# Kernel optimization log

Measured on AMD Instinct MI355X. Metric: run time of the kernel, lower is better.

## Reference

```python
import jax, jax.numpy as jnp
import numpy as np

B, N, DIM, H, DH = 8, 1024, 1024, 16, 64

def setup_inputs() -> dict:
    key = jax.random.key(0)
    ks = jax.random.split(key, 6)
    return {
        'x': jax.random.normal(ks[0], (B, N, DIM), dtype=jnp.float32),
        'freqs': jax.random.normal(ks[1], (1, N, DH), dtype=jnp.float32),
        'bias': jax.random.normal(ks[2], (1, N, DH), dtype=jnp.float32),
        'ln_gamma': jnp.ones((DIM,), jnp.float32),
        'ln_beta': jnp.zeros((DIM,), jnp.float32),
        'w_qk': jax.random.normal(ks[3], (DIM, 2 * H * DH), dtype=jnp.float32) * (DIM ** -0.5),
        'w_v': jax.random.normal(ks[4], (DIM, H * DH), dtype=jnp.float32) * (DIM ** -0.5),
        'w_out': jax.random.normal(ks[5], (H * DH, DIM), dtype=jnp.float32) * ((H * DH) ** -0.5),
        'b_out': jnp.zeros((DIM,), jnp.float32),
    }

def _apply_polar(t, freqs):
    # t: [b,h,n,d]; freqs: [1,n,d] broadcast over b,h. Output doubles last dim.
    t = jax.nn.softplus(t)
    return jnp.concatenate((t * jnp.cos(freqs), t * jnp.sin(freqs)), axis=-1)

def reference(x, freqs, bias, ln_gamma, ln_beta, w_qk, w_v, w_out, b_out):
    eps = 1e-5
    mu = jnp.mean(x, axis=-1, keepdims=True)
    var = jnp.var(x, axis=-1, keepdims=True)
    xn = (x - mu) * jax.lax.rsqrt(var + eps) * ln_gamma + ln_beta
    qk = jnp.einsum('bnd,de->bne', xn, w_qk)
    q, k = jnp.split(qk, 2, axis=-1)
    v = jnp.einsum('bnd,de->bne', xn, w_v)
    split_heads = lambda t: t.reshape(B, N, H, DH).transpose(0, 2, 1, 3)
    q, k, v = split_heads(q), split_heads(k), split_heads(v)
    q = _apply_polar(q, freqs)          # [b,h,n,2*DH]
    k = _apply_polar(k, freqs + bias)   # [b,h,n,2*DH]
    scale = DH ** -0.5
    dots = jnp.einsum('bhnd,bhmd->bhnm', q, k) * scale
    attn = jax.nn.softmax(dots, axis=-1)
    out = jnp.einsum('bhnm,bhmd->bhnd', attn, v)
    out = out.transpose(0, 2, 1, 3).reshape(B, N, H * DH)
    return jnp.einsum('bne,ed->bnd', out, w_out) + b_out
```

## Files before the change

### kernel.cpp

```cpp
#include <hip/hip_runtime.h>
#include <cmath>

using f16   = _Float16;
using f16x2 = __attribute__((ext_vector_type(2))) _Float16;
using f16x4 = __attribute__((ext_vector_type(4))) _Float16;
using f16x8 = __attribute__((ext_vector_type(8))) _Float16;
using f32x4 = __attribute__((ext_vector_type(4))) float;

#define DEV __device__ __forceinline__

constexpr int Bb  = 8;
constexpr int Nn  = 1024;
constexpr int DIM = 1024;
constexpr int Hh  = 16;
constexpr int DH  = 64;
constexpr int EQKV = 3072;

DEV void async16(const f16* g, f16* l) {
  __builtin_amdgcn_global_load_lds(
      (const __attribute__((address_space(1))) void*)g,
      (__attribute__((address_space(3))) void*)l, 16, 0, 0);
}

DEV float softplusf(float x) {
  return fmaxf(x, 0.f) + __logf(1.f + __expf(-fabsf(x)));
}

__global__ __launch_bounds__(256) void transpose_cvt3(const float* __restrict__ s0,
                                                      const float* __restrict__ s1,
                                                      const float* __restrict__ s2,
                                                      f16* __restrict__ d0,
                                                      f16* __restrict__ d2) {
  __shared__ float tile[32][33];
  const float* src; f16* dst; int cols;
  int bz = blockIdx.z;
  if (bz == 0)      { src = s0; dst = d0;                        cols = 2048; }
  else if (bz == 1) { src = s1; dst = d0 + (size_t)2048 * 1024;  cols = 1024; }
  else              { src = s2; dst = d2;                        cols = 1024; }
  int c0 = blockIdx.x * 32, r0 = blockIdx.y * 32;
  if (c0 >= cols) return;
  int t = threadIdx.x, tx = t & 31, ty = t >> 5;
#pragma unroll
  for (int j = 0; j < 32; j += 8)
    tile[ty + j][tx] = src[(size_t)(r0 + ty + j) * cols + c0 + tx];
  __syncthreads();
#pragma unroll
  for (int j = 0; j < 32; j += 8)
    dst[(size_t)(c0 + ty + j) * 1024 + r0 + tx] = (f16)tile[tx][ty + j];
}

__global__ __launch_bounds__(256) void ln_kernel(const float* __restrict__ x,
                                                 const float* __restrict__ gamma,
                                                 const float* __restrict__ beta,
                                                 f16* __restrict__ xn) {
  int row = blockIdx.x;
  int t = threadIdx.x;
  const float4* xr = (const float4*)(x + (size_t)row * DIM);
  float4 v = xr[t];
  float s  = v.x + v.y + v.z + v.w;
  float s2 = v.x * v.x + v.y * v.y + v.z * v.z + v.w * v.w;
#pragma unroll
  for (int off = 32; off; off >>= 1) {
    s  += __shfl_xor(s,  off, 64);
    s2 += __shfl_xor(s2, off, 64);
  }
  __shared__ float red[8];
  int wv = t >> 6, lane = t & 63;
  if (lane == 0) { red[wv] = s; red[4 + wv] = s2; }
  __syncthreads();
  s  = red[0] + red[1] + red[2] + red[3];
  s2 = red[4] + red[5] + red[6] + red[7];
  float mu  = s * (1.f / DIM);
  float var = s2 * (1.f / DIM) - mu * mu;
  float rs  = rsqrtf(var + 1e-5f);
  float4 g = ((const float4*)gamma)[t];
  float4 bb = ((const float4*)beta)[t];
  f16x4 o;
  o[0] = (f16)((v.x - mu) * rs * g.x + bb.x);
  o[1] = (f16)((v.y - mu) * rs * g.y + bb.y);
  o[2] = (f16)((v.z - mu) * rs * g.z + bb.z);
  o[3] = (f16)((v.w - mu) * rs * g.w + bb.w);
  ((f16x4*)(xn + (size_t)row * DIM))[t] = o;
}

template <bool FP32OUT>
__global__ __launch_bounds__(256) void gemm_bt(const f16* __restrict__ A,
                                               const f16* __restrict__ Bt,
                                               void* __restrict__ Cv,
                                               const float* __restrict__ bias,
                                               int M, int K, int E) {
  __shared__ f16 lA[128 * 32];
  __shared__ f16 lB[128 * 32];
  int tid  = threadIdx.x;
  int lane = tid & 63;
  int wv   = __builtin_amdgcn_readfirstlane(tid >> 6);
  int nbe  = E >> 7;
  int bm = blockIdx.x / nbe, be = blockIdx.x % nbe;
  size_t m0 = (size_t)bm * 128, e0 = (size_t)be * 128;
  int wm = (wv & 1) * 64, we = (wv >> 1) * 64;
  int lm = lane & 15, q = lane >> 4;

  f32x4 acc[4][4] = {};

  int row_s[2], cg_s[2];
#pragma unroll
  for (int r = 0; r < 2; ++r) {
    int s = r * 256 + tid;
    row_s[r] = s >> 2;
    cg_s[r]  = (s & 3) ^ ((row_s[r] >> 1) & 3);
  }
  const f16* pa[4];
  const f16* pb[4];
#pragma unroll
  for (int i = 0; i < 4; ++i) {
    int ra = wm + i * 16 + lm;
    pa[i] = lA + ra * 32 + (q ^ ((ra >> 1) & 3)) * 8;
    int rb = we + i * 16 + lm;
    pb[i] = lB + rb * 32 + (q ^ ((rb >> 1) & 3)) * 8;
  }

  for (int k0 = 0; k0 < K; k0 += 32) {
#pragma unroll
    for (int r = 0; r < 2; ++r) {
      const f16* ga = A  + (m0 + row_s[r]) * K + k0 + cg_s[r] * 8;
      const f16* gb = Bt + (e0 + row_s[r]) * K + k0 + cg_s[r] * 8;
      async16(ga, lA + (r * 256 + wv * 64) * 8);
      async16(gb, lB + (r * 256 + wv * 64) * 8);
    }
    __syncthreads();
    f16x8 af[4], bf[4];
#pragma unroll
    for (int i = 0; i < 4; ++i) {
      af[i] = *(const f16x8*)pa[i];
      bf[i] = *(const f16x8*)pb[i];
    }
#pragma unroll
    for (int i = 0; i < 4; ++i)
#pragma unroll
      for (int j = 0; j < 4; ++j)
        acc[i][j] = __builtin_amdgcn_mfma_f32_16x16x32_f16(af[i], bf[j], acc[i][j], 0, 0, 0);
    __syncthreads();
  }

#pragma unroll
  for (int i = 0; i < 4; ++i) {
    size_t mbase = m0 + wm + i * 16 + q * 4;
#pragma unroll
    for (int j = 0; j < 4; ++j) {
      size_t e = e0 + we + j * 16 + lm;
#pragma unroll
      for (int g = 0; g < 4; ++g) {
        float val = acc[i][j][g];
        if (FP32OUT)
          ((float*)Cv)[(mbase + g) * (size_t)E + e] = val + bias[e];
        else
          ((f16*)Cv)[(mbase + g) * (size_t)E + e] = (f16)val;
      }
    }
  }
}

template <bool FP32OUT>
__global__ __launch_bounds__(512, 2) void gemm256(const f16* __restrict__ A,
                                                  const f16* __restrict__ Bt,
                                                  void* __restrict__ Cv,
                                                  const float* __restrict__ bias,
                                                  int M, int K, int E) {
  __shared__ f16 sm[65536];
  const int tid  = threadIdx.x;
  const int lane = tid & 63;
  const int wv   = __builtin_amdgcn_readfirstlane(tid >> 6);
  const int lm   = lane & 15, q = lane >> 4;
  const int wrow = (wv >> 2) * 128;
  const int wcol = (wv & 3) * 64;

  const int nbe = E >> 8;
  const int cpx = gridDim.x >> 3;
  const int bid = blockIdx.x;
  const int swz = (bid & 7) * cpx + (bid >> 3);
  const int bm = swz / nbe, be = swz % nbe;
  const size_t m0 = (size_t)bm * 256, e0 = (size_t)be * 256;

  const int rl  = lane >> 3;
  const int pcp = lane & 7;
  const int cg  = pcp ^ rl;
  const f16* aS = A  + (m0 + (size_t)(wv * 8 + rl)) * K + cg * 8;
  const f16* bS = Bt + (e0 + (size_t)((wv >> 2) * 64 + (wv & 3) * 8 + rl)) * K + cg * 8;
  const int aDofs = wv * 512;
  const int bDofs = 16384 + ((wv >> 2) * 64 + (wv & 3) * 8) * 64;

  const int x0 = ((0 + q) ^ (lm & 7)) * 8;
  const int x1 = ((4 + q) ^ (lm & 7)) * 8;

  const int NT = K >> 6;

  async16(aS,                     sm + aDofs);
  async16(aS + (size_t)64 * K,    sm + aDofs + 64 * 64);
  async16(aS + (size_t)128 * K,   sm + aDofs + 128 * 64);
  async16(aS + (size_t)192 * K,   sm + aDofs + 192 * 64);
  async16(bS,                     sm + bDofs);
  async16(bS + (size_t)32 * K,    sm + bDofs + 32 * 64);
  async16(bS + (size_t)128 * K,   sm + bDofs + 128 * 64);
  async16(bS + (size_t)160 * K,   sm + bDofs + 160 * 64);

  f32x4 acc[8][4] = {};
  f16x8 af[4][2], bf[4][2];

  for (int t = 0; t < NT; ++t) {
    const int b = t & 1, nb = b ^ 1;
    const int tn = (t + 1 < NT) ? t + 1 : t;
    const f16* pA = sm + b * 32768;
    const f16* pB = pA + 16384;
    f16* aD = sm + nb * 32768 + aDofs;
    f16* bD = sm + nb * 32768 + bDofs;
    const f16* aSk = aS + tn * 64;
    const f16* bSk = bS + tn * 64;

    __builtin_amdgcn_s_barrier();

    async16(aSk,                   aD);
    async16(aSk + (size_t)64 * K,  aD + 64 * 64);
    async16(aSk + (size_t)128 * K, aD + 128 * 64);
    async16(aSk + (size_t)192 * K, aD + 192 * 64);
    async16(bSk,                   bD);
    async16(bSk + (size_t)32 * K,  bD + 32 * 64);
    async16(bSk + (size_t)128 * K, bD + 128 * 64);
    async16(bSk + (size_t)160 * K, bD + 160 * 64);

    asm volatile("s_waitcnt vmcnt(8)" ::: "memory");
    __builtin_amdgcn_s_barrier();

#pragma unroll
    for (int i = 0; i < 4; ++i) {
      const f16* p = pA + (wrow + i * 16 + lm) * 64;
      af[i][0] = *(const f16x8*)(p + x0);
      af[i][1] = *(const f16x8*)(p + x1);
    }
#pragma unroll
    for (int j = 0; j < 2; ++j) {
      const f16* p = pB + (wcol + j * 16 + lm) * 64;
      bf[j][0] = *(const f16x8*)(p + x0);
      bf[j][1] = *(const f16x8*)(p + x1);
    }
    __builtin_amdgcn_s_setprio(1);
#pragma unroll
    for (int i = 0; i < 4; ++i)
#pragma unroll
      for (int j = 0; j < 2; ++j) {
        acc[i][j] = __builtin_amdgcn_mfma_f32_16x16x32_f16(af[i][0], bf[j][0], acc[i][j], 0, 0, 0);
        acc[i][j] = __builtin_amdgcn_mfma_f32_16x16x32_f16(af[i][1], bf[j][1], acc[i][j], 0, 0, 0);
      }
    __builtin_amdgcn_s_setprio(0);
    __builtin_amdgcn_s_barrier();

#pragma unroll
    for (int j = 0; j < 2; ++j) {
      const f16* p = pB + (wcol + 32 + j * 16 + lm) * 64;
      bf[2 + j][0] = *(const f16x8*)(p + x0);
      bf[2 + j][1] = *(const f16x8*)(p + x1);
    }
    __builtin_amdgcn_s_setprio(1);
#pragma unroll
    for (int i = 0; i < 4; ++i)
#pragma unroll
      for (int j = 2; j < 4; ++j) {
        acc[i][j] = __builtin_amdgcn_mfma_f32_16x16x32_f16(af[i][0], bf[j][0], acc[i][j], 0, 0, 0);
        acc[i][j] = __builtin_amdgcn_mfma_f32_16x16x32_f16(af[i][1], bf[j][1], acc[i][j], 0, 0, 0);
      }
    __builtin_amdgcn_s_setprio(0);
    __builtin_amdgcn_s_barrier();

#pragma unroll
    for (int i = 0; i < 4; ++i) {
      const f16* p = pA + (wrow + 64 + i * 16 + lm) * 64;
      af[i][0] = *(const f16x8*)(p + x0);
      af[i][1] = *(const f16x8*)(p + x1);
    }
    __builtin_amdgcn_s_setprio(1);
#pragma unroll
    for (int i = 0; i < 4; ++i)
#pragma unroll
      for (int j = 0; j < 2; ++j) {
        acc[4 + i][j] = __builtin_amdgcn_mfma_f32_16x16x32_f16(af[i][0], bf[j][0], acc[4 + i][j], 0, 0, 0);
        acc[4 + i][j] = __builtin_amdgcn_mfma_f32_16x16x32_f16(af[i][1], bf[j][1], acc[4 + i][j], 0, 0, 0);
      }
    __builtin_amdgcn_s_setprio(0);
    __builtin_amdgcn_s_barrier();

    __builtin_amdgcn_s_setprio(1);
#pragma unroll
    for (int i = 0; i < 4; ++i)
#pragma unroll
      for (int j = 2; j < 4; ++j) {
        acc[4 + i][j] = __builtin_amdgcn_mfma_f32_16x16x32_f16(af[i][0], bf[j][0], acc[4 + i][j], 0, 0, 0);
        acc[4 + i][j] = __builtin_amdgcn_mfma_f32_16x16x32_f16(af[i][1], bf[j][1], acc[4 + i][j], 0, 0, 0);
      }
    __builtin_amdgcn_s_setprio(0);
  }
  asm volatile("s_waitcnt vmcnt(0)" ::: "memory");

#pragma unroll
  for (int ii = 0; ii < 8; ++ii) {
    size_t mrow = m0 + wrow + (ii >> 2) * 64 + (ii & 3) * 16 + q * 4;
#pragma unroll
    for (int j = 0; j < 4; ++j) {
      size_t e = e0 + wcol + j * 16 + lm;
#pragma unroll
      for (int g = 0; g < 4; ++g) {
        float val = acc[ii][j][g];
        if (FP32OUT)
          ((float*)Cv)[(mrow + g) * (size_t)E + e] = val + bias[e];
        else
          ((f16*)Cv)[(mrow + g) * (size_t)E + e] = (f16)val;
      }
    }
  }
}

__global__ __launch_bounds__(256) void polar_kernel(const f16* __restrict__ qkv,
                                                    const float* __restrict__ freqs,
                                                    const float* __restrict__ fbias,
                                                    f16* __restrict__ Qp,
                                                    f16* __restrict__ Kp,
                                                    f16* __restrict__ Vt) {
  __shared__ f16 vt[64 * 66];
  int tid = threadIdx.x;
  int bx = blockIdx.x;
  int nt = bx & 15, bh = bx >> 4;
  int b = bh >> 4, h = bh & 15;
  size_t tok0 = (size_t)b * Nn + nt * 64;
  int n0 = nt * 64;
  constexpr float kScale = 0.125f;
#pragma unroll
  for (int i = 0; i < 8; ++i) {
    int e2 = tid + i * 256;
    int nl = e2 >> 5, dp = (e2 & 31) * 2;
    size_t src = (tok0 + nl) * EQKV + h * 64 + dp;
    f16x2 q2 = *(const f16x2*)(qkv + src);
    f16x2 k2 = *(const f16x2*)(qkv + src + 1024);
    f16x2 v2 = *(const f16x2*)(qkv + src + 2048);
    int fidx = (n0 + nl) * 64 + dp;
    float2 f2  = *(const float2*)(freqs + fidx);
    float2 fb2 = *(const float2*)(fbias + fidx);
    f16x2 qc, qs, kc, ksn;
#pragma unroll
    for (int u = 0; u < 2; ++u) {
      float fq = u ? f2.y : f2.x;
      float fk = fq + (u ? fb2.y : fb2.x);
      float spq = softplusf((float)q2[u]) * kScale;
      float spk = softplusf((float)k2[u]);
      float snq, csq, snk, csk;
      __sincosf(fq, &snq, &csq);
      __sincosf(fk, &snk, &csk);
      qc[u]  = (f16)(spq * csq);
      qs[u]  = (f16)(spq * snq);
      kc[u]  = (f16)(spk * csk);
      ksn[u] = (f16)(spk * snk);
    }
    size_t dst = ((size_t)bh * Nn + n0 + nl) * 128 + dp;
    *(f16x2*)(Qp + dst)      = qc;
    *(f16x2*)(Qp + dst + 64) = qs;
    *(f16x2*)(Kp + dst)      = kc;
    *(f16x2*)(Kp + dst + 64) = ksn;
    vt[dp * 66 + nl]       = v2[0];
    vt[(dp + 1) * 66 + nl] = v2[1];
  }
  __syncthreads();
#pragma unroll
  for (int i = 0; i < 16; ++i) {
    int e = tid + i * 256;
    int d = e >> 6, nl = e & 63;
    Vt[((size_t)bh * 64 + d) * Nn + n0 + nl] = vt[d * 66 + nl];
  }
}

constexpr int VK0 = 0;
constexpr int VK1 = 8192;
constexpr int VV0 = 16384;
constexpr int VV1 = 21504;
constexpr int VEND = 26624;

__global__ __launch_bounds__(256, 3) void attn_kernel(const f16* __restrict__ Qp,
                                                      const f16* __restrict__ Kp,
                                                      const f16* __restrict__ Vt,
                                                      f16* __restrict__ attout) {
  __shared__ f16 smem[VEND];

  int tid = threadIdx.x, lane = tid & 63;
  int wv = __builtin_amdgcn_readfirstlane(tid >> 6);
  int lm = lane & 15, q = lane >> 4;
  int bx = blockIdx.x;
  int bh = (bx & 7) | ((bx >> 6) << 3);
  int qt = (bx >> 3) & 7;
  const f16* Kbase = Kp + (size_t)bh * Nn * 128;
  const f16* Vbase = Vt + (size_t)bh * 64 * Nn;

  {
    int idx = tid * 4;
    f16 val = (idx < 64) ? (f16)1.0f : (f16)0.0f;
    f16x4 v4 = {val, val, val, val};
    *(f16x4*)(smem + VV0 + 64 * 64 + idx) = v4;
    *(f16x4*)(smem + VV1 + 64 * 64 + idx) = v4;
  }

#pragma unroll
  for (int i = 0; i < 4; ++i) {
    int s = i * 256 + tid;
    int r = s >> 4, c = s & 15;
    int g = c ^ (r & 15);
    async16(Kbase + (size_t)r * 128 + g * 8, smem + VK0 + (i * 256 + wv * 64) * 8);
  }
#pragma unroll
  for (int i = 0; i < 2; ++i) {
    int s = i * 256 + tid;
    int r = s >> 3, c = s & 7;
    int g = c ^ (r & 7);
    async16(Vbase + (size_t)r * Nn + g * 8, smem + VV0 + (i * 256 + wv * 64) * 8);
  }

  f16x8 qf[2][4];
  {
    const f16* Qb = Qp + ((size_t)bh * Nn + qt * 128 + wv * 32) * 128;
#pragma unroll
    for (int grp = 0; grp < 2; ++grp)
#pragma unroll
      for (int ks = 0; ks < 4; ++ks)
        qf[grp][ks] = *(const f16x8*)(Qb + (size_t)(grp * 16 + lm) * 128 + ks * 32 + q * 8);
  }

  f32x4 O[2][5] = {};
  float mrow[2] = {-INFINITY, -INFINITY};

  for (int kt = 0; kt < 16; ++kt) {
    __syncthreads();

    if (kt < 15) {
      f16* nK = smem + ((kt & 1) ? VK0 : VK1);
      f16* nV = smem + ((kt & 1) ? VV0 : VV1);
#pragma unroll
      for (int i = 0; i < 4; ++i) {
        int s = i * 256 + tid;
        int r = s >> 4, c = s & 15;
        int g = c ^ (r & 15);
        async16(Kbase + (size_t)((kt + 1) * 64 + r) * 128 + g * 8, nK + (i * 256 + wv * 64) * 8);
      }
#pragma unroll
      for (int i = 0; i < 2; ++i) {
        int s = i * 256 + tid;
        int r = s >> 3, c = s & 7;
        int g = c ^ (r & 7);
        async16(Vbase + (size_t)r * Nn + (kt + 1) * 64 + g * 8, nV + (i * 256 + wv * 64) * 8);
      }
    }
    const f16* sK = smem + ((kt & 1) ? VK1 : VK0);
    const f16* sV = smem + ((kt & 1) ? VV1 : VV0);

    f32x4 S[2][4] = {};
    __builtin_amdgcn_s_setprio(1);
#pragma unroll
    for (int nt = 0; nt < 4; ++nt) {
      f16x8 kf[4];
#pragma unroll
      for (int ks = 0; ks < 4; ++ks)
        kf[ks] = *(const f16x8*)(sK + (nt * 16 + lm) * 128 + (((ks * 4 + q) ^ lm) * 8));
#pragma unroll
      for (int ks = 0; ks < 4; ++ks) {
        S[0][nt] = __builtin_amdgcn_mfma_f32_16x16x32_f16(kf[ks], qf[0][ks], S[0][nt], 0, 0, 0);
        S[1][nt] = __builtin_amdgcn_mfma_f32_16x16x32_f16(kf[ks], qf[1][ks], S[1][nt], 0, 0, 0);
      }
    }
    __builtin_amdgcn_s_setprio(0);

    f16x4 pf[2][4];
#pragma unroll
    for (int grp = 0; grp < 2; ++grp) {
      float mx = -INFINITY;
#pragma unroll
      for (int nt = 0; nt < 4; ++nt)
#pragma unroll
        for (int g = 0; g < 4; ++g) mx = fmaxf(mx, S[grp][nt][g]);
      mx = fmaxf(mx, __shfl_xor(mx, 16, 64));
      mx = fmaxf(mx, __shfl_xor(mx, 32, 64));
      float mn = fmaxf(mrow[grp], mx);
      float alpha = __expf(mrow[grp] - mn);
      mrow[grp] = mn;
#pragma unroll
      for (int nt = 0; nt < 4; ++nt)
#pragma unroll
        for (int g = 0; g < 4; ++g)
          pf[grp][nt][g] = (f16)__expf(S[grp][nt][g] - mn);
#pragma unroll
      for (int nto = 0; nto < 5; ++nto)
#pragma unroll
        for (int g = 0; g < 4; ++g) O[grp][nto][g] *= alpha;
    }

    __builtin_amdgcn_s_setprio(1);
#pragma unroll
    for (int nto = 0; nto < 5; ++nto) {
      int r = nto * 16 + lm;
#pragma unroll
      for (int nt = 0; nt < 4; ++nt) {
        int c16 = (nt * 2 + (q >> 1)) ^ (r & 7);
        f16x4 vf = *(const f16x4*)(sV + r * 64 + c16 * 8 + (q & 1) * 4);
        O[0][nto] = __builtin_amdgcn_mfma_f32_16x16x16f16(vf, pf[0][nt], O[0][nto], 0, 0, 0);
        O[1][nto] = __builtin_amdgcn_mfma_f32_16x16x16f16(vf, pf[1][nt], O[1][nto], 0, 0, 0);
      }
    }
    __builtin_amdgcn_s_setprio(0);
  }

  int b = bh >> 4, h = bh & 15;
#pragma unroll
  for (int grp = 0; grp < 2; ++grp) {
    float l = __shfl(O[grp][4][0], lm, 64);
    float inv = 1.f / l;
    size_t token = (size_t)b * Nn + qt * 128 + wv * 32 + grp * 16 + lm;
#pragma unroll
    for (int nto = 0; nto < 4; ++nto) {
      f16x4 o4;
#pragma unroll
      for (int g = 0; g < 4; ++g) o4[g] = (f16)(O[grp][nto][g] * inv);
      *(f16x4*)(attout + token * (size_t)(Hh * DH) + h * 64 + nto * 16 + q * 4) = o4;
    }
  }
}

extern "C" void kernel_launch(void* const* d_in, const int* in_sizes, int n_in,
                              void* d_out, int out_size, void* d_ws, size_t ws_size,
                              hipStream_t stream) {
  const float* x     = (const float*)d_in[0];
  const float* freqs = (const float*)d_in[1];
  const float* fbias = (const float*)d_in[2];
  const float* gamma = (const float*)d_in[3];
  const float* beta  = (const float*)d_in[4];
  const float* w_qk  = (const float*)d_in[5];
  const float* w_v   = (const float*)d_in[6];
  const float* w_out = (const float*)d_in[7];
  const float* b_out = (const float*)d_in[8];
  float* out = (float*)d_out;

  const size_t T = (size_t)Bb * Nn;
  f16* WqkvT = (f16*)d_ws;
  f16* WoutT = WqkvT + (size_t)EQKV * DIM;
  f16* Xn    = WoutT + (size_t)DIM * DIM;
  f16* QKV   = Xn + T * DIM;
  f16* AttO  = QKV + T * EQKV;
  f16* Qp    = AttO + T * DIM;
  f16* Kp    = Qp + (size_t)128 * Nn * 128;
  f16* Vt    = Kp + (size_t)128 * Nn * 128;

  transpose_cvt3<<<dim3(64, 32, 3), 256, 0, stream>>>(w_qk, w_v, w_out, WqkvT, WoutT);

  ln_kernel<<<(int)T, 256, 0, stream>>>(x, gamma, beta, Xn);

  gemm256<false><<<(int)(T / 256) * (EQKV / 256), 512, 0, stream>>>(
      Xn, WqkvT, (void*)QKV, nullptr, (int)T, DIM, EQKV);

  polar_kernel<<<Bb * Hh * (Nn / 64), 256, 0, stream>>>(QKV, freqs, fbias, Qp, Kp, Vt);

  attn_kernel<<<Bb * Hh * (Nn / 128), 256, 0, stream>>>(Qp, Kp, Vt, AttO);

  gemm_bt<true><<<(int)(T / 128) * (DIM / 128), 256, 0, stream>>>(
      AttO, WoutT, (void*)out, b_out, (int)T, DIM, DIM);
}
```

Measured before the change: 310.5 us.

## Fuse softplus-polar transform into QKV GEMM epilogue with precomputed trig table

Softplus and the polar cos/sin expansion of Q and K now run directly in the QKV GEMM epilogue. The GEMM writes Q and K in their final per-head layout, with cos/sin pairs interleaved instead of split into halves. This removes the round trip of Q and K through a separate intermediate buffer and the standalone polar kernel. A small kernel precomputes the cos/sin tables once, V is written to its own buffer and transposed by a slimmed kernel, and the s_setprio hints are dropped from the attention loop. In exchange, the epilogue stores are scattered 4-byte writes, and there is one extra small launch.

```diff
diff --git a/kernel.cpp b/kernel.cpp
--- a/kernel.cpp
+++ b/kernel.cpp
@@ -47,6 +47,17 @@
 #pragma unroll
   for (int j = 0; j < 32; j += 8)
     dst[(size_t)(c0 + ty + j) * 1024 + r0 + tx] = (f16)tile[tx][ty + j];
+}
+
+__global__ __launch_bounds__(256) void trig_prep(const float* __restrict__ freqs,
+                                                 const float* __restrict__ fbias,
+                                                 float4* __restrict__ trig) {
+  int i = blockIdx.x * 256 + threadIdx.x;
+  float f = freqs[i], fb = fbias[i];
+  float cq, sq, ck, sk;
+  __sincosf(f, &sq, &cq);
+  __sincosf(f + fb, &sk, &ck);
+  trig[i] = make_float4(cq, sq, ck, sk);
 }
 
 __global__ __launch_bounds__(256) void ln_kernel(const float* __restrict__ x,
@@ -160,12 +171,13 @@
   }
 }
 
-template <bool FP32OUT>
-__global__ __launch_bounds__(512, 2) void gemm256(const f16* __restrict__ A,
-                                                  const f16* __restrict__ Bt,
-                                                  void* __restrict__ Cv,
-                                                  const float* __restrict__ bias,
-                                                  int M, int K, int E) {
+__global__ __launch_bounds__(512, 2) void gemm_qkv(const f16* __restrict__ A,
+                                                   const f16* __restrict__ Bt,
+                                                   f16* __restrict__ Qp,
+                                                   f16* __restrict__ Kp,
+                                                   f16* __restrict__ Vn,
+                                                   const float4* __restrict__ trig,
+                                                   int M, int K) {
   __shared__ f16 sm[65536];
   const int tid  = threadIdx.x;
   const int lane = tid & 63;
@@ -174,7 +186,7 @@
   const int wrow = (wv >> 2) * 128;
   const int wcol = (wv & 3) * 64;
 
-  const int nbe = E >> 8;
+  const int nbe = EQKV >> 8;
   const int cpx = gridDim.x >> 3;
   const int bid = blockIdx.x;
   const int swz = (bid & 7) * cpx + (bid >> 3);
@@ -299,30 +311,48 @@
   }
   asm volatile("s_waitcnt vmcnt(0)" ::: "memory");
 
-#pragma unroll
-  for (int ii = 0; ii < 8; ++ii) {
-    size_t mrow = m0 + wrow + (ii >> 2) * 64 + (ii & 3) * 16 + q * 4;
-#pragma unroll
-    for (int j = 0; j < 4; ++j) {
-      size_t e = e0 + wcol + j * 16 + lm;
-#pragma unroll
-      for (int g = 0; g < 4; ++g) {
-        float val = acc[ii][j][g];
-        if (FP32OUT)
-          ((float*)Cv)[(mrow + g) * (size_t)E + e] = val + bias[e];
-        else
-          ((f16*)Cv)[(mrow + g) * (size_t)E + e] = (f16)val;
-      }
-    }
-  }
-}
-
-__global__ __launch_bounds__(256) void polar_kernel(const f16* __restrict__ qkv,
-                                                    const float* __restrict__ freqs,
-                                                    const float* __restrict__ fbias,
-                                                    f16* __restrict__ Qp,
-                                                    f16* __restrict__ Kp,
-                                                    f16* __restrict__ Vt) {
+  const int sec = be >> 2;
+  if (sec < 2) {
+    f16* dst = (sec == 0) ? Qp : Kp;
+    const float scl = (sec == 0) ? 0.125f : 1.0f;
+#pragma unroll
+    for (int ii = 0; ii < 8; ++ii) {
+      size_t mrow = m0 + wrow + (ii >> 2) * 64 + (ii & 3) * 16 + q * 4;
+#pragma unroll
+      for (int j = 0; j < 4; ++j) {
+        int hd = (int)((e0 + wcol + j * 16 + lm) & 1023);
+        int h = hd >> 6, d = hd & 63;
+#pragma unroll
+        for (int g = 0; g < 4; ++g) {
+          size_t tok = mrow + g;
+          int n = (int)(tok & 1023);
+          size_t bh = (tok >> 10) * 16 + h;
+          float sp = softplusf(acc[ii][j][g]) * scl;
+          float4 T = trig[n * 64 + d];
+          float c = (sec == 0) ? T.x : T.z;
+          float s = (sec == 0) ? T.y : T.w;
+          f16x2 o = { (f16)(sp * c), (f16)(sp * s) };
+          *(f16x2*)(dst + (bh * (size_t)Nn + n) * 128 + 2 * d) = o;
+        }
+      }
+    }
+  } else {
+#pragma unroll
+    for (int ii = 0; ii < 8; ++ii) {
+      size_t mrow = m0 + wrow + (ii >> 2) * 64 + (ii & 3) * 16 + q * 4;
+#pragma unroll
+      for (int j = 0; j < 4; ++j) {
+        int hd = (int)((e0 + wcol + j * 16 + lm) & 1023);
+#pragma unroll
+        for (int g = 0; g < 4; ++g)
+          Vn[(mrow + g) * 1024 + hd] = (f16)acc[ii][j][g];
+      }
+    }
+  }
+}
+
+__global__ __launch_bounds__(256) void vtrans_kernel(const f16* __restrict__ Vn,
+                                                     f16* __restrict__ Vt) {
   __shared__ f16 vt[64 * 66];
   int tid = threadIdx.x;
   int bx = blockIdx.x;
@@ -330,38 +360,11 @@
   int b = bh >> 4, h = bh & 15;
   size_t tok0 = (size_t)b * Nn + nt * 64;
   int n0 = nt * 64;
-  constexpr float kScale = 0.125f;
 #pragma unroll
   for (int i = 0; i < 8; ++i) {
     int e2 = tid + i * 256;
     int nl = e2 >> 5, dp = (e2 & 31) * 2;
-    size_t src = (tok0 + nl) * EQKV + h * 64 + dp;
-    f16x2 q2 = *(const f16x2*)(qkv + src);
-    f16x2 k2 = *(const f16x2*)(qkv + src + 1024);
-    f16x2 v2 = *(const f16x2*)(qkv + src + 2048);
-    int fidx = (n0 + nl) * 64 + dp;
-    float2 f2  = *(const float2*)(freqs + fidx);
-    float2 fb2 = *(const float2*)(fbias + fidx);
-    f16x2 qc, qs, kc, ksn;
-#pragma unroll
-    for (int u = 0; u < 2; ++u) {
-      float fq = u ? f2.y : f2.x;
-      float fk = fq + (u ? fb2.y : fb2.x);
-      float spq = softplusf((float)q2[u]) * kScale;
-      float spk = softplusf((float)k2[u]);
-      float snq, csq, snk, csk;
-      __sincosf(fq, &snq, &csq);
-      __sincosf(fk, &snk, &csk);
-      qc[u]  = (f16)(spq * csq);
-      qs[u]  = (f16)(spq * snq);
-      kc[u]  = (f16)(spk * csk);
-      ksn[u] = (f16)(spk * snk);
-    }
-    size_t dst = ((size_t)bh * Nn + n0 + nl) * 128 + dp;
-    *(f16x2*)(Qp + dst)      = qc;
-    *(f16x2*)(Qp + dst + 64) = qs;
-    *(f16x2*)(Kp + dst)      = kc;
-    *(f16x2*)(Kp + dst + 64) = ksn;
+    f16x2 v2 = *(const f16x2*)(Vn + (tok0 + nl) * 1024 + h * 64 + dp);
     vt[dp * 66 + nl]       = v2[0];
     vt[(dp + 1) * 66 + nl] = v2[1];
   }
@@ -456,7 +459,6 @@
     const f16* sV = smem + ((kt & 1) ? VV1 : VV0);
 
     f32x4 S[2][4] = {};
-    __builtin_amdgcn_s_setprio(1);
 #pragma unroll
     for (int nt = 0; nt < 4; ++nt) {
       f16x8 kf[4];
@@ -469,7 +471,6 @@
         S[1][nt] = __builtin_amdgcn_mfma_f32_16x16x32_f16(kf[ks], qf[1][ks], S[1][nt], 0, 0, 0);
       }
     }
-    __builtin_amdgcn_s_setprio(0);
 
     f16x4 pf[2][4];
 #pragma unroll
@@ -495,7 +496,6 @@
         for (int g = 0; g < 4; ++g) O[grp][nto][g] *= alpha;
     }
 
-    __builtin_amdgcn_s_setprio(1);
 #pragma unroll
     for (int nto = 0; nto < 5; ++nto) {
       int r = nto * 16 + lm;
@@ -507,7 +507,6 @@
         O[1][nto] = __builtin_amdgcn_mfma_f32_16x16x16f16(vf, pf[1][nt], O[1][nto], 0, 0, 0);
       }
     }
-    __builtin_amdgcn_s_setprio(0);
   }
 
   int b = bh >> 4, h = bh & 15;
@@ -543,21 +542,24 @@
   const size_t T = (size_t)Bb * Nn;
   f16* WqkvT = (f16*)d_ws;
   f16* WoutT = WqkvT + (size_t)EQKV * DIM;
-  f16* Xn    = WoutT + (size_t)DIM * DIM;
-  f16* QKV   = Xn + T * DIM;
-  f16* AttO  = QKV + T * EQKV;
+  float4* trig = (float4*)(WoutT + (size_t)DIM * DIM);
+  f16* Xn    = (f16*)(trig + (size_t)Nn * DH);
+  f16* Vn    = Xn + T * DIM;
+  f16* AttO  = Vn + T * DIM;
   f16* Qp    = AttO + T * DIM;
   f16* Kp    = Qp + (size_t)128 * Nn * 128;
   f16* Vt    = Kp + (size_t)128 * Nn * 128;
 
   transpose_cvt3<<<dim3(64, 32, 3), 256, 0, stream>>>(w_qk, w_v, w_out, WqkvT, WoutT);
 
+  trig_prep<<<(Nn * DH) / 256, 256, 0, stream>>>(freqs, fbias, trig);
+
   ln_kernel<<<(int)T, 256, 0, stream>>>(x, gamma, beta, Xn);
 
-  gemm256<false><<<(int)(T / 256) * (EQKV / 256), 512, 0, stream>>>(
-      Xn, WqkvT, (void*)QKV, nullptr, (int)T, DIM, EQKV);
-
-  polar_kernel<<<Bb * Hh * (Nn / 64), 256, 0, stream>>>(QKV, freqs, fbias, Qp, Kp, Vt);
+  gemm_qkv<<<(int)(T / 256) * (EQKV / 256), 512, 0, stream>>>(
+      Xn, WqkvT, Qp, Kp, Vn, trig, (int)T, DIM);
+
+  vtrans_kernel<<<Bb * Hh * (Nn / 64), 256, 0, stream>>>(Vn, Vt);
 
   attn_kernel<<<Bb * Hh * (Nn / 128), 256, 0, stream>>>(Qp, Kp, Vt, AttO);
 
```

Result: faster. 295.0 us (-5.0%).
